# Performance work log

Measured on AMD Instinct MI355X. Metric: run time of the kernel, lower is better.

## Reference

```python
import jax, jax.numpy as jnp
import numpy as np
import math


def _attn(q, k, v):
    # q,k,v: [B, S, d] (d == 1 here). bmm -> scale -> softmax -> bmm.
    scale = 1.0 / math.sqrt(q.shape[2])
    e = jnp.einsum('bsd,btd->bst', q, k) * scale  # [B, S, S]
    w = jax.nn.softmax(e, axis=2)
    return jnp.einsum('bst,btd->bsd', w, v)


def setup_inputs() -> dict:
    key = jax.random.key(0)
    ks = jax.random.split(key, 12)
    B, D = 32, 768
    CLF_OUT = 7
    inp = {}
    names = ['sentence', 'target_spkr_snts', 'other_spkr_snts', 'scene_desc', 'scene_sent']
    for i, name in enumerate(names):
        inp[name] = jax.random.normal(ks[i], (B, D), dtype=jnp.float32)
    inp['W_shared'] = jax.random.normal(ks[5], (768, 512), dtype=jnp.float32) * 0.02
    inp['b_shared'] = jnp.zeros((512,), dtype=jnp.float32)
    inp['W1'] = jax.random.normal(ks[6], (3840, 256), dtype=jnp.float32) * 0.02
    inp['b1'] = jnp.zeros((256,), dtype=jnp.float32)
    inp['W2'] = jax.random.normal(ks[7], (256, CLF_OUT), dtype=jnp.float32) * 0.02
    inp['b2'] = jnp.zeros((CLF_OUT,), dtype=jnp.float32)
    return inp


def reference(sentence, target_spkr_snts, other_spkr_snts, scene_desc, scene_sent,
              W_shared, b_shared, W1, b1, W2, b2):
    B = sentence.shape[0]
    s = sentence[..., None]             # [B, 768, 1]
    sd = scene_desc[..., None]
    ts = target_spkr_snts[..., None]
    oth = other_spkr_snts[..., None]
    ss = scene_sent[..., None]

    speaker_context = _attn(oth, ts, ts)   # [B, 768, 1]
    scene_context = _attn(ss, ss, sd)      # [B, 768, 1]

    sentence_shared = sentence @ W_shared + b_shared                     # [B, 512]
    scene_context_shared = scene_context.reshape(B, -1) @ W_shared + b_shared
    speaker_context_shared = speaker_context.reshape(B, -1) @ W_shared + b_shared

    fused = jnp.concatenate([s, scene_context, speaker_context], axis=1)  # [B, 2304, 1]
    z = _attn(fused, fused, fused)                                        # [B, 2304, 1]

    final = jnp.concatenate([z.reshape(B, -1), sentence_shared,
                             scene_context_shared, speaker_context_shared], axis=1)  # [B, 3840]
    h = jax.nn.relu(final @ W1 + b1)   # dropout is identity in eval mode
    return jax.nn.sigmoid(h @ W2 + b2)  # [B, 7]
```

## Files before the change

kernel.cpp:

```cpp
#include <hip/hip_runtime.h>
#include <math.h>

#define NPOW 80
#define NCO  72


__device__ __forceinline__ float red64f(float x) {
    x += __shfl_xor(x, 1, 64);
    x += __shfl_xor(x, 2, 64);
    x += __shfl_xor(x, 4, 64);
    x += __shfl_xor(x, 8, 64);
    x += __shfl_xor(x, 16, 64);
    x += __shfl_xor(x, 32, 64);
    return x;
}

__device__ __forceinline__ void scan768_S(const float* __restrict__ x,
                                          float* __restrict__ partS, int tid) {
    const int w = tid >> 6, lane = tid & 63;
    float pw[12], g4[12];
    #pragma unroll
    for (int e = 0; e < 12; ++e) {
        const float g  = x[lane + 64 * e] * 0.25f;
        const float g2 = g * g;
        g4[e] = g2 * g2;
        pw[e] = (w == 0) ? 1.f : ((w == 1) ? g : ((w == 2) ? g2 : g2 * g));
    }
    for (int i = 0; i < 19; ++i) {
        float s = ((pw[0] + pw[1]) + (pw[2] + pw[3]))
                + ((pw[4] + pw[5]) + (pw[6] + pw[7]))
                + ((pw[8] + pw[9]) + (pw[10] + pw[11]));
        s = red64f(s);
        if (lane == 0) partS[w + 4 * i] = s;
        #pragma unroll
        for (int e = 0; e < 12; ++e) pw[e] *= g4[e];
    }
}

__device__ __forceinline__ void scan768_ST(const float* __restrict__ x,
                                           const float* __restrict__ v,
                                           float* __restrict__ partS,
                                           float* __restrict__ partT, int tid) {
    const int w = tid >> 6, lane = tid & 63;
    float pw[12], g4[12], vv[12];
    #pragma unroll
    for (int e = 0; e < 12; ++e) {
        const float g  = x[lane + 64 * e] * 0.25f;
        const float g2 = g * g;
        g4[e] = g2 * g2;
        pw[e] = (w == 0) ? 1.f : ((w == 1) ? g : ((w == 2) ? g2 : g2 * g));
        vv[e] = v[lane + 64 * e];
    }
    for (int i = 0; i < 19; ++i) {
        float s = ((pw[0] + pw[1]) + (pw[2] + pw[3]))
                + ((pw[4] + pw[5]) + (pw[6] + pw[7]))
                + ((pw[8] + pw[9]) + (pw[10] + pw[11]));
        float t = ((pw[0]*vv[0] + pw[1]*vv[1]) + (pw[2]*vv[2] + pw[3]*vv[3]))
                + ((pw[4]*vv[4] + pw[5]*vv[5]) + (pw[6]*vv[6] + pw[7]*vv[7]))
                + ((pw[8]*vv[8] + pw[9]*vv[9]) + (pw[10]*vv[10] + pw[11]*vv[11]));
        s = red64f(s);
        t = red64f(t);
        if (lane == 0) { partS[w + 4 * i] = s; partT[w + 4 * i] = t; }
        #pragma unroll
        for (int e = 0; e < 12; ++e) pw[e] *= g4[e];
    }
}

__device__ __forceinline__ void proj_256(
    const float* __restrict__ xsrc,
    const float* __restrict__ Ws,
    const float* __restrict__ bs,
    float* __restrict__ dst,
    float* xb,
    float* redf,
    int tid)
{
    for (int i = tid; i < 768; i += 256) xb[i] = xsrc[i];
    __syncthreads();

    const int g = tid >> 7;
    const int q = tid & 127;
    const float4* __restrict__ Wv = (const float4*)Ws;
    float ax = 0.f, ay = 0.f, az = 0.f, aw = 0.f;
    #pragma unroll 8
    for (int k = g; k < 768; k += 2) {
        const float xv = xb[k];
        const float4 w = Wv[k * 128 + q];
        ax += xv * w.x; ay += xv * w.y; az += xv * w.z; aw += xv * w.w;
    }
    redf[g * 512 + q * 4 + 0] = ax;
    redf[g * 512 + q * 4 + 1] = ay;
    redf[g * 512 + q * 4 + 2] = az;
    redf[g * 512 + q * 4 + 3] = aw;
    __syncthreads();

    dst[tid]       = bs[tid]       + redf[tid]       + redf[512 + tid];
    dst[tid + 256] = bs[tid + 256] + redf[tid + 256] + redf[512 + tid + 256];
}

__global__ __launch_bounds__(256) void k1_small_kernel(
    const float* __restrict__ sentence,
    const float* __restrict__ target,
    const float* __restrict__ other,
    const float* __restrict__ scene_desc,
    const float* __restrict__ scene_sent,
    const float* __restrict__ Ws,
    const float* __restrict__ bs,
    float* __restrict__ ctx,
    float* __restrict__ final_)
{
    const int b = blockIdx.x, y = blockIdx.y, tid = threadIdx.x;
    __shared__ float xb[768];
    __shared__ float vbuf[768];
    __shared__ float partS[NPOW];
    __shared__ float partT[NPOW];
    __shared__ double coefA[NCO];
    __shared__ double coefB[NCO];
    __shared__ float redf[1024];

    if (y == 2) {
        proj_256(sentence + b * 768, Ws, bs, final_ + b * 3840 + 2304, xb, redf, tid);
        return;
    }

    const bool scene = (y == 0);
    const float* kp = scene ? (scene_sent + b * 768) : (target + b * 768);
    for (int i = tid; i < 768; i += 256) xb[i] = kp[i];
    if (scene)
        for (int i = tid; i < 768; i += 256) vbuf[i] = scene_desc[b * 768 + i];
    __syncthreads();
    if (scene) scan768_ST(xb, vbuf, partS, partT, tid);
    else       scan768_S(xb, partS, tid);
    __syncthreads();

    if (tid < NCO) {
        double fact = 1.0;
        for (int i = 2; i <= tid; ++i) fact *= (double)i;
        const double inv = 1.0 / fact;
        coefA[tid] = (double)partS[tid] * inv;
        coefB[tid] = scene ? ((double)partT[tid] * inv)
                           : ((double)partS[tid + 1] * inv);
    }
    __syncthreads();

    double q[3], num[3], den[3];
    #pragma unroll
    for (int j = 0; j < 3; ++j) {
        const int r = tid + 256 * j;
        q[j] = 4.0 * (double)(scene ? xb[r] : other[b * 768 + r]);
        den[j] = coefA[NCO - 1];
        num[j] = coefB[NCO - 1];
    }
    for (int n = NCO - 2; n >= 0; --n) {
        const double a = coefA[n], cc = coefB[n];
        #pragma unroll
        for (int j = 0; j < 3; ++j) {
            den[j] = fma(den[j], q[j], a);
            num[j] = fma(num[j], q[j], cc);
        }
    }
    #pragma unroll
    for (int j = 0; j < 3; ++j) {
        const double ratio = scene ? (num[j] / den[j]) : (4.0 * num[j] / den[j]);
        ctx[b * 1536 + (scene ? 0 : 768) + tid + 256 * j] = (float)ratio;
    }
}

__global__ __launch_bounds__(256) void k2_fused_kernel(
    const float* __restrict__ sentence,
    const float* __restrict__ ctx,
    const float* __restrict__ Ws,
    const float* __restrict__ bs,
    float* __restrict__ final_)
{
    const int b = blockIdx.x, y = blockIdx.y, tid = threadIdx.x;
    __shared__ float fb[2304];
    __shared__ float redbuf[2][2048];
    __shared__ float partS[NPOW];
    __shared__ double coefA[NCO];
    __shared__ double coefB[NCO];
    __shared__ float redf[1024];

    if (y >= 9) {
        const int p = y - 8;
        proj_256(ctx + b * 1536 + (p - 1) * 768, Ws, bs,
                 final_ + b * 3840 + 2304 + p * 512, fb, redf, tid);
        return;
    }

    for (int i = tid; i < 2304; i += 256)
        fb[i] = (i < 768) ? sentence[b * 768 + i] : ctx[b * 1536 + (i - 768)];
    __syncthreads();

    float g[9], pw[9];
    #pragma unroll
    for (int j = 0; j < 9; ++j) { g[j] = fb[tid + 256 * j] * 0.25f; pw[j] = 1.f; }

    for (int c = 0; c < 10; ++c) {
        float* buf = redbuf[c & 1];
        #pragma unroll
        for (int m = 0; m < 8; ++m) {
            buf[m * 256 + tid] = (((pw[0] + pw[1]) + (pw[2] + pw[3]))
                                + ((pw[4] + pw[5]) + (pw[6] + pw[7]))) + pw[8];
            #pragma unroll
            for (int j = 0; j < 9; ++j) pw[j] *= g[j];
        }
        __syncthreads();
        const int n = tid >> 5, l = tid & 31;
        const float* src = buf + n * 256 + l;
        float acc = ((src[0] + src[32]) + (src[64] + src[96]))
                  + ((src[128] + src[160]) + (src[192] + src[224]));
        acc += __shfl_xor(acc, 1, 64);
        acc += __shfl_xor(acc, 2, 64);
        acc += __shfl_xor(acc, 4, 64);
        acc += __shfl_xor(acc, 8, 64);
        acc += __shfl_xor(acc, 16, 64);
        if (l == 0) partS[c * 8 + n] = acc;
    }
    __syncthreads();

    if (tid < NCO) {
        double fact = 1.0;
        for (int i = 2; i <= tid; ++i) fact *= (double)i;
        const double inv = 1.0 / fact;
        coefA[tid] = (double)partS[tid] * inv;
        coefB[tid] = (double)partS[tid + 1] * inv;
    }
    __syncthreads();

    const int r = y * 256 + tid;
    const double x = 4.0 * (double)fb[r];
    double den = coefA[NCO - 1], num = coefB[NCO - 1];
    for (int n = NCO - 2; n >= 0; --n) {
        den = fma(den, x, coefA[n]);
        num = fma(num, x, coefB[n]);
    }
    final_[b * 3840 + r] = (float)(4.0 * num / den);
}

__global__ __launch_bounds__(1024) void mlp_part_kernel(
    const float* __restrict__ final_,
    const float* __restrict__ W1,
    float* __restrict__ hpart)
{
    const int b = blockIdx.x;
    const int c = blockIdx.y;
    const int tid = threadIdx.x;
    const int base = c * 480;

    __shared__ float fb[480];
    __shared__ float red[16][256];
    if (tid < 480) fb[tid] = final_[b * 3840 + base + tid];
    __syncthreads();

    const int g = tid >> 6;
    const int q = tid & 63;
    const float4* __restrict__ Wv = (const float4*)W1;
    float ax = 0.f, ay = 0.f, az = 0.f, aw = 0.f;
    const int l0 = g * 30;
    #pragma unroll 5
    for (int kk = 0; kk < 30; ++kk) {
        const float xv = fb[l0 + kk];
        const float4 w = Wv[(base + l0 + kk) * 64 + q];
        ax += xv * w.x; ay += xv * w.y; az += xv * w.z; aw += xv * w.w;
    }
    red[g][q * 4 + 0] = ax;
    red[g][q * 4 + 1] = ay;
    red[g][q * 4 + 2] = az;
    red[g][q * 4 + 3] = aw;
    __syncthreads();

    if (tid < 256) {
        float s = 0.f;
        #pragma unroll
        for (int g2 = 0; g2 < 16; ++g2) s += red[g2][tid];
        hpart[(b * 8 + c) * 256 + tid] = s;
    }
}

__global__ __launch_bounds__(512) void mlp_tail_kernel(
    const float* __restrict__ hpart,
    const float* __restrict__ b1,
    const float* __restrict__ W2,
    const float* __restrict__ b2,
    float* __restrict__ out)
{
    const int b = blockIdx.x;
    const int tid = threadIdx.x;

    __shared__ float hb[256];
    if (tid < 256) {
        float s = b1[tid];
        #pragma unroll
        for (int c = 0; c < 8; ++c) s += hpart[(b * 8 + c) * 256 + tid];
        hb[tid] = fmaxf(s, 0.f);
    }
    __syncthreads();

    const int w = tid >> 6;
    const int lane = tid & 63;
    if (w < 7) {
        float a = 0.f;
        #pragma unroll
        for (int c = lane; c < 256; c += 64)
            a += hb[c] * W2[c * 7 + w];
        #pragma unroll
        for (int off = 32; off > 0; off >>= 1)
            a += __shfl_down(a, off, 64);
        if (lane == 0)
            out[b * 7 + w] = 1.f / (1.f + __expf(-(a + b2[w])));
    }
}

extern "C" void kernel_launch(void* const* d_in, const int* in_sizes, int n_in,
                              void* d_out, int out_size, void* d_ws, size_t ws_size,
                              hipStream_t stream) {
    const float* sentence   = (const float*)d_in[0];
    const float* target     = (const float*)d_in[1];
    const float* other      = (const float*)d_in[2];
    const float* scene_desc = (const float*)d_in[3];
    const float* scene_sent = (const float*)d_in[4];
    const float* Ws         = (const float*)d_in[5];
    const float* bs         = (const float*)d_in[6];
    const float* W1         = (const float*)d_in[7];
    const float* b1         = (const float*)d_in[8];
    const float* W2         = (const float*)d_in[9];
    const float* b2         = (const float*)d_in[10];
    float* out = (float*)d_out;

    float* ctx    = (float*)d_ws;
    float* final_ = ctx + 32 * 1536;
    float* hpart  = final_ + 32 * 3840;

    k1_small_kernel<<<dim3(32, 3), 256, 0, stream>>>(sentence, target, other,
                                                     scene_desc, scene_sent,
                                                     Ws, bs, ctx, final_);
    k2_fused_kernel<<<dim3(32, 11), 256, 0, stream>>>(sentence, ctx, Ws, bs, final_);
    mlp_part_kernel<<<dim3(32, 8), 1024, 0, stream>>>(final_, W1, hpart);
    mlp_tail_kernel<<<32, 512, 0, stream>>>(hpart, b1, W2, b2, out);
}
```

Baseline: 50.47 us.

## Precompute power-sum moments in k1 and batch four rows per MLP block

```diff
diff --git a/kernel.cpp b/kernel.cpp
--- a/kernel.cpp
+++ b/kernel.cpp
@@ -1,7 +1,7 @@
 #include <hip/hip_runtime.h>
 #include <math.h>
 
-#define NPOW 80
+#define MOMN 76
 #define NCO  72
 
 
@@ -66,38 +66,6 @@
     }
 }
 
-__device__ __forceinline__ void proj_256(
-    const float* __restrict__ xsrc,
-    const float* __restrict__ Ws,
-    const float* __restrict__ bs,
-    float* __restrict__ dst,
-    float* xb,
-    float* redf,
-    int tid)
-{
-    for (int i = tid; i < 768; i += 256) xb[i] = xsrc[i];
-    __syncthreads();
-
-    const int g = tid >> 7;
-    const int q = tid & 127;
-    const float4* __restrict__ Wv = (const float4*)Ws;
-    float ax = 0.f, ay = 0.f, az = 0.f, aw = 0.f;
-    #pragma unroll 8
-    for (int k = g; k < 768; k += 2) {
-        const float xv = xb[k];
-        const float4 w = Wv[k * 128 + q];
-        ax += xv * w.x; ay += xv * w.y; az += xv * w.z; aw += xv * w.w;
-    }
-    redf[g * 512 + q * 4 + 0] = ax;
-    redf[g * 512 + q * 4 + 1] = ay;
-    redf[g * 512 + q * 4 + 2] = az;
-    redf[g * 512 + q * 4 + 3] = aw;
-    __syncthreads();
-
-    dst[tid]       = bs[tid]       + redf[tid]       + redf[512 + tid];
-    dst[tid + 256] = bs[tid + 256] + redf[tid + 256] + redf[512 + tid + 256];
-}
-
 __global__ __launch_bounds__(256) void k1_small_kernel(
     const float* __restrict__ sentence,
     const float* __restrict__ target,
@@ -107,19 +75,43 @@
     const float* __restrict__ Ws,
     const float* __restrict__ bs,
     float* __restrict__ ctx,
+    float* __restrict__ mom,
     float* __restrict__ final_)
 {
     const int b = blockIdx.x, y = blockIdx.y, tid = threadIdx.x;
     __shared__ float xb[768];
     __shared__ float vbuf[768];
-    __shared__ float partS[NPOW];
-    __shared__ float partT[NPOW];
+    __shared__ float partS[MOMN];
+    __shared__ float partT[MOMN];
     __shared__ double coefA[NCO];
     __shared__ double coefB[NCO];
     __shared__ float redf[1024];
 
     if (y == 2) {
-        proj_256(sentence + b * 768, Ws, bs, final_ + b * 3840 + 2304, xb, redf, tid);
+        for (int i = tid; i < 768; i += 256) xb[i] = sentence[b * 768 + i];
+        __syncthreads();
+        scan768_S(xb, partS, tid);
+
+        const int g = tid >> 7;
+        const int q = tid & 127;
+        const float4* __restrict__ Wv = (const float4*)Ws;
+        float ax = 0.f, ay = 0.f, az = 0.f, aw = 0.f;
+        #pragma unroll 8
+        for (int k = g; k < 768; k += 2) {
+            const float xv = xb[k];
+            const float4 w = Wv[k * 128 + q];
+            ax += xv * w.x; ay += xv * w.y; az += xv * w.z; aw += xv * w.w;
+        }
+        redf[g * 512 + q * 4 + 0] = ax;
+        redf[g * 512 + q * 4 + 1] = ay;
+        redf[g * 512 + q * 4 + 2] = az;
+        redf[g * 512 + q * 4 + 3] = aw;
+        __syncthreads();
+
+        float* dst = final_ + b * 3840 + 2304;
+        dst[tid]       = bs[tid]       + redf[tid]       + redf[512 + tid];
+        dst[tid + 256] = bs[tid + 256] + redf[tid + 256] + redf[512 + tid + 256];
+        if (tid < MOMN) mom[(b * 3 + 0) * MOMN + tid] = partS[tid];
         return;
     }
 
@@ -161,9 +153,14 @@
     }
     #pragma unroll
     for (int j = 0; j < 3; ++j) {
-        const double ratio = scene ? (num[j] / den[j]) : (4.0 * num[j] / den[j]);
-        ctx[b * 1536 + (scene ? 0 : 768) + tid + 256 * j] = (float)ratio;
-    }
+        const float cv = (float)(scene ? (num[j] / den[j]) : (4.0 * num[j] / den[j]));
+        ctx[b * 1536 + (scene ? 0 : 768) + tid + 256 * j] = cv;
+        vbuf[tid + 256 * j] = cv;
+    }
+    __syncthreads();
+    scan768_S(vbuf, partS, tid);
+    __syncthreads();
+    if (tid < MOMN) mom[(b * 3 + (scene ? 1 : 2)) * MOMN + tid] = partS[tid];
 }
 
 __global__ __launch_bounds__(256) void k2_fused_kernel(
@@ -171,54 +168,47 @@
     const float* __restrict__ ctx,
     const float* __restrict__ Ws,
     const float* __restrict__ bs,
+    const float* __restrict__ mom,
     float* __restrict__ final_)
 {
     const int b = blockIdx.x, y = blockIdx.y, tid = threadIdx.x;
-    __shared__ float fb[2304];
-    __shared__ float redbuf[2][2048];
-    __shared__ float partS[NPOW];
+    __shared__ float partS[MOMN];
     __shared__ double coefA[NCO];
     __shared__ double coefB[NCO];
+    __shared__ float xb[768];
     __shared__ float redf[1024];
 
     if (y >= 9) {
         const int p = y - 8;
-        proj_256(ctx + b * 1536 + (p - 1) * 768, Ws, bs,
-                 final_ + b * 3840 + 2304 + p * 512, fb, redf, tid);
+        const float* xsrc = ctx + b * 1536 + (p - 1) * 768;
+        for (int i = tid; i < 768; i += 256) xb[i] = xsrc[i];
+        __syncthreads();
+        const int g = tid >> 7;
+        const int q = tid & 127;
+        const float4* __restrict__ Wv = (const float4*)Ws;
+        float ax = 0.f, ay = 0.f, az = 0.f, aw = 0.f;
+        #pragma unroll 8
+        for (int k = g; k < 768; k += 2) {
+            const float xv = xb[k];
+            const float4 w = Wv[k * 128 + q];
+            ax += xv * w.x; ay += xv * w.y; az += xv * w.z; aw += xv * w.w;
+        }
+        redf[g * 512 + q * 4 + 0] = ax;
+        redf[g * 512 + q * 4 + 1] = ay;
+        redf[g * 512 + q * 4 + 2] = az;
+        redf[g * 512 + q * 4 + 3] = aw;
+        __syncthreads();
+        float* dst = final_ + b * 3840 + 2304 + p * 512;
+        dst[tid]       = bs[tid]       + redf[tid]       + redf[512 + tid];
+        dst[tid + 256] = bs[tid + 256] + redf[tid + 256] + redf[512 + tid + 256];
         return;
     }
 
-    for (int i = tid; i < 2304; i += 256)
-        fb[i] = (i < 768) ? sentence[b * 768 + i] : ctx[b * 1536 + (i - 768)];
-    __syncthreads();
-
-    float g[9], pw[9];
-    #pragma unroll
-    for (int j = 0; j < 9; ++j) { g[j] = fb[tid + 256 * j] * 0.25f; pw[j] = 1.f; }
-
-    for (int c = 0; c < 10; ++c) {
-        float* buf = redbuf[c & 1];
-        #pragma unroll
-        for (int m = 0; m < 8; ++m) {
-            buf[m * 256 + tid] = (((pw[0] + pw[1]) + (pw[2] + pw[3]))
-                                + ((pw[4] + pw[5]) + (pw[6] + pw[7]))) + pw[8];
-            #pragma unroll
-            for (int j = 0; j < 9; ++j) pw[j] *= g[j];
-        }
-        __syncthreads();
-        const int n = tid >> 5, l = tid & 31;
-        const float* src = buf + n * 256 + l;
-        float acc = ((src[0] + src[32]) + (src[64] + src[96]))
-                  + ((src[128] + src[160]) + (src[192] + src[224]));
-        acc += __shfl_xor(acc, 1, 64);
-        acc += __shfl_xor(acc, 2, 64);
-        acc += __shfl_xor(acc, 4, 64);
-        acc += __shfl_xor(acc, 8, 64);
-        acc += __shfl_xor(acc, 16, 64);
-        if (l == 0) partS[c * 8 + n] = acc;
-    }
-    __syncthreads();
-
+    if (tid < MOMN)
+        partS[tid] = mom[(b * 3 + 0) * MOMN + tid]
+                   + mom[(b * 3 + 1) * MOMN + tid]
+                   + mom[(b * 3 + 2) * MOMN + tid];
+    __syncthreads();
     if (tid < NCO) {
         double fact = 1.0;
         for (int i = 2; i <= tid; ++i) fact *= (double)i;
@@ -229,7 +219,8 @@
     __syncthreads();
 
     const int r = y * 256 + tid;
-    const double x = 4.0 * (double)fb[r];
+    const float fq = (r < 768) ? sentence[b * 768 + r] : ctx[b * 1536 + (r - 768)];
+    const double x = 4.0 * (double)fq;
     double den = coefA[NCO - 1], num = coefB[NCO - 1];
     for (int n = NCO - 2; n >= 0; --n) {
         den = fma(den, x, coefA[n]);
@@ -238,44 +229,63 @@
     final_[b * 3840 + r] = (float)(4.0 * num / den);
 }
 
-__global__ __launch_bounds__(1024) void mlp_part_kernel(
+__global__ __launch_bounds__(1024) void mlp_b_kernel(
     const float* __restrict__ final_,
     const float* __restrict__ W1,
     float* __restrict__ hpart)
 {
-    const int b = blockIdx.x;
-    const int c = blockIdx.y;
+    const int bg = blockIdx.x;
+    const int c  = blockIdx.y;
     const int tid = threadIdx.x;
     const int base = c * 480;
 
-    __shared__ float fb[480];
+    __shared__ float act[4][480];
     __shared__ float red[16][256];
-    if (tid < 480) fb[tid] = final_[b * 3840 + base + tid];
-    __syncthreads();
-
-    const int g = tid >> 6;
-    const int q = tid & 63;
-    const float4* __restrict__ Wv = (const float4*)W1;
-    float ax = 0.f, ay = 0.f, az = 0.f, aw = 0.f;
-    const int l0 = g * 30;
-    #pragma unroll 5
-    for (int kk = 0; kk < 30; ++kk) {
-        const float xv = fb[l0 + kk];
-        const float4 w = Wv[(base + l0 + kk) * 64 + q];
-        ax += xv * w.x; ay += xv * w.y; az += xv * w.z; aw += xv * w.w;
-    }
-    red[g][q * 4 + 0] = ax;
-    red[g][q * 4 + 1] = ay;
-    red[g][q * 4 + 2] = az;
-    red[g][q * 4 + 3] = aw;
-    __syncthreads();
-
-    if (tid < 256) {
-        float s = 0.f;
-        #pragma unroll
-        for (int g2 = 0; g2 < 16; ++g2) s += red[g2][tid];
-        hpart[(b * 8 + c) * 256 + tid] = s;
-    }
+
+    for (int i = tid; i < 4 * 480; i += 1024) {
+        const int bb = i / 480, k = i - bb * 480;
+        act[bb][k] = final_[(4 * bg + bb) * 3840 + base + k];
+    }
+    __syncthreads();
+
+    const int col = tid & 255;
+    const int kg  = tid >> 8;
+    const float4* __restrict__ a0 = (const float4*)act[0];
+    const float4* __restrict__ a1 = (const float4*)act[1];
+    const float4* __restrict__ a2 = (const float4*)act[2];
+    const float4* __restrict__ a3 = (const float4*)act[3];
+    float acc0 = 0.f, acc1 = 0.f, acc2 = 0.f, acc3 = 0.f;
+    const int k0 = kg * 120;
+    #pragma unroll 2
+    for (int j = 0; j < 120; j += 4) {
+        const int k = k0 + j;
+        const float4 v0 = a0[k >> 2];
+        const float4 v1 = a1[k >> 2];
+        const float4 v2 = a2[k >> 2];
+        const float4 v3 = a3[k >> 2];
+        const float w0 = W1[(base + k + 0) * 256 + col];
+        const float w1 = W1[(base + k + 1) * 256 + col];
+        const float w2 = W1[(base + k + 2) * 256 + col];
+        const float w3 = W1[(base + k + 3) * 256 + col];
+        acc0 = fmaf(v0.x, w0, acc0); acc0 = fmaf(v0.y, w1, acc0);
+        acc0 = fmaf(v0.z, w2, acc0); acc0 = fmaf(v0.w, w3, acc0);
+        acc1 = fmaf(v1.x, w0, acc1); acc1 = fmaf(v1.y, w1, acc1);
+        acc1 = fmaf(v1.z, w2, acc1); acc1 = fmaf(v1.w, w3, acc1);
+        acc2 = fmaf(v2.x, w0, acc2); acc2 = fmaf(v2.y, w1, acc2);
+        acc2 = fmaf(v2.z, w2, acc2); acc2 = fmaf(v2.w, w3, acc2);
+        acc3 = fmaf(v3.x, w0, acc3); acc3 = fmaf(v3.y, w1, acc3);
+        acc3 = fmaf(v3.z, w2, acc3); acc3 = fmaf(v3.w, w3, acc3);
+    }
+    red[kg * 4 + 0][col] = acc0;
+    red[kg * 4 + 1][col] = acc1;
+    red[kg * 4 + 2][col] = acc2;
+    red[kg * 4 + 3][col] = acc3;
+    __syncthreads();
+
+    const int bb = tid >> 8;
+    float s = red[0 * 4 + bb][col] + red[1 * 4 + bb][col]
+            + red[2 * 4 + bb][col] + red[3 * 4 + bb][col];
+    hpart[((4 * bg + bb) * 8 + c) * 256 + col] = s;
 }
 
 __global__ __launch_bounds__(512) void mlp_tail_kernel(
@@ -329,13 +339,14 @@
     float* out = (float*)d_out;
 
     float* ctx    = (float*)d_ws;
-    float* final_ = ctx + 32 * 1536;
+    float* mom    = ctx + 32 * 1536;
+    float* final_ = mom + 32 * 3 * MOMN;
     float* hpart  = final_ + 32 * 3840;
 
     k1_small_kernel<<<dim3(32, 3), 256, 0, stream>>>(sentence, target, other,
                                                      scene_desc, scene_sent,
-                                                     Ws, bs, ctx, final_);
-    k2_fused_kernel<<<dim3(32, 11), 256, 0, stream>>>(sentence, ctx, Ws, bs, final_);
-    mlp_part_kernel<<<dim3(32, 8), 1024, 0, stream>>>(final_, W1, hpart);
+                                                     Ws, bs, ctx, mom, final_);
+    k2_fused_kernel<<<dim3(32, 11), 256, 0, stream>>>(sentence, ctx, Ws, bs, mom, final_);
+    mlp_b_kernel<<<dim3(8, 8), 1024, 0, stream>>>(final_, W1, hpart);
     mlp_tail_kernel<<<32, 512, 0, stream>>>(hpart, b1, W2, b2, out);
 }
```

Measured after the change: 56.54 us. 1.12x slower.
